# Kernel optimization log

Measured on AMD Instinct MI355X. Metric: run time of the kernel, lower is better.

## Reference

```python
import jax, jax.numpy as jnp
import numpy as np

N_FEAT = 256
N_HID = 128
N_HEAD = 4
N_HEAD_LAST = 6
N_CLASS = 40
NEG_SLOPE = 0.2


def gat_conv(x, src, dst, W, att_src, att_dst, bias, heads, ch, concat):
    # x: [N, in], W: [in, heads*ch], att_*: [heads, ch]
    N = x.shape[0]
    xw = (x @ W).reshape(N, heads, ch)                      # [N, H, C]
    a_src = jnp.sum(xw * att_src, axis=-1)                  # [N, H]
    a_dst = jnp.sum(xw * att_dst, axis=-1)                  # [N, H]
    e = jax.nn.leaky_relu(a_src[src] + a_dst[dst], NEG_SLOPE)  # [E, H]
    # softmax over incoming edges of each destination node
    m = jax.ops.segment_max(e, dst, num_segments=N)         # [N, H]
    ex = jnp.exp(e - m[dst])
    denom = jax.ops.segment_sum(ex, dst, num_segments=N)    # [N, H]
    alpha = ex / (denom[dst] + 1e-16)                       # [E, H]
    msg = xw[src] * alpha[..., None]                        # [E, H, C]
    out = jax.ops.segment_sum(msg, dst, num_segments=N)     # [N, H, C]
    out = out.reshape(N, heads * ch) if concat else out.mean(axis=1)
    return out + bias


def setup_inputs() -> dict:
    key = jax.random.key(0)
    ks = jax.random.split(key, 16)
    N, E = 10000, 160000
    x = jax.random.normal(ks[0], (N, N_FEAT), dtype=jnp.float32)
    edge_index = jax.random.randint(ks[1], (2, E), 0, N, dtype=jnp.int64)
    hid = N_HID * N_HEAD  # 512
    s = lambda fan: 1.0 / np.sqrt(fan)
    return {
        "x": x,
        "edge_index": edge_index,
        "W0": jax.random.normal(ks[2], (N_FEAT, hid), jnp.float32) * s(N_FEAT),
        "a_src0": jax.random.normal(ks[3], (N_HEAD, N_HID), jnp.float32) * s(N_HID),
        "a_dst0": jax.random.normal(ks[4], (N_HEAD, N_HID), jnp.float32) * s(N_HID),
        "b0": jnp.zeros((hid,), jnp.float32),
        "Wskip_in": jax.random.normal(ks[5], (N_FEAT, hid), jnp.float32) * s(N_FEAT),
        "W1": jax.random.normal(ks[6], (hid, hid), jnp.float32) * s(hid),
        "a_src1": jax.random.normal(ks[7], (N_HEAD, N_HID), jnp.float32) * s(N_HID),
        "a_dst1": jax.random.normal(ks[8], (N_HEAD, N_HID), jnp.float32) * s(N_HID),
        "b1": jnp.zeros((hid,), jnp.float32),
        "W2": jax.random.normal(ks[9], (hid, N_HEAD_LAST * N_CLASS), jnp.float32) * s(hid),
        "a_src2": jax.random.normal(ks[10], (N_HEAD_LAST, N_CLASS), jnp.float32) * s(N_CLASS),
        "a_dst2": jax.random.normal(ks[11], (N_HEAD_LAST, N_CLASS), jnp.float32) * s(N_CLASS),
        "b2": jnp.zeros((N_CLASS,), jnp.float32),
        "Wskip_out": jax.random.normal(ks[12], (hid, N_CLASS), jnp.float32) * s(hid),
    }


def reference(x, edge_index, W0, a_src0, a_dst0, b0, Wskip_in,
              W1, a_src1, a_dst1, b1,
              W2, a_src2, a_dst2, b2, Wskip_out):
    N = x.shape[0]
    loops = jnp.arange(N, dtype=edge_index.dtype)
    src = jnp.concatenate([edge_index[0], loops])  # add self loops (PyG GATConv)
    dst = jnp.concatenate([edge_index[1], loops])
    # eval mode: dropout is identity
    h = gat_conv(x, src, dst, W0, a_src0, a_dst0, b0, N_HEAD, N_HID, True)
    x1 = jax.nn.elu(h + x @ Wskip_in)                      # res skip w/ projection
    h = gat_conv(x1, src, dst, W1, a_src1, a_dst1, b1, N_HEAD, N_HID, True)
    x2 = jax.nn.elu(h + x1)                                # res skip, same dims
    h = gat_conv(x2, src, dst, W2, a_src2, a_dst2, b2, N_HEAD_LAST, N_CLASS, False)
    out = h + x2 @ Wskip_out                               # out_skip 'res'
    return out
```

## Files before the change

### kernel.cpp

```cpp
#include <hip/hip_runtime.h>
#include <math.h>


#define N_FEAT 256
#define HID 512

using u16 = unsigned short;
using bf16x8 = __attribute__((ext_vector_type(8))) __bf16;
using f32x16 = __attribute__((ext_vector_type(16))) float;

__device__ inline u16 bf16_rne(float f) {
    unsigned u = __float_as_uint(f);
    return (u16)((u + 0x7fffu + ((u >> 16) & 1u)) >> 16);
}
__device__ inline float bf16_to_f32(u16 h) {
    return __uint_as_float((unsigned)h << 16);
}
__device__ inline bf16x8 ldb8(const u16* p) {
    return *reinterpret_cast<const bf16x8*>(p);
}
__device__ inline void acc8(float a, const uint4 r, float* acc) {
    acc[0] = fmaf(a, __uint_as_float(r.x << 16), acc[0]);
    acc[1] = fmaf(a, __uint_as_float(r.x & 0xffff0000u), acc[1]);
    acc[2] = fmaf(a, __uint_as_float(r.y << 16), acc[2]);
    acc[3] = fmaf(a, __uint_as_float(r.y & 0xffff0000u), acc[3]);
    acc[4] = fmaf(a, __uint_as_float(r.z << 16), acc[4]);
    acc[5] = fmaf(a, __uint_as_float(r.z & 0xffff0000u), acc[5]);
    acc[6] = fmaf(a, __uint_as_float(r.w << 16), acc[6]);
    acc[7] = fmaf(a, __uint_as_float(r.w & 0xffff0000u), acc[7]);
}


__global__ void init_counts(int* cursor, int N) {
    int i = blockIdx.x * blockDim.x + threadIdx.x;
    if (i < N) cursor[i] = 1;
}

__global__ void count_edges(const int* __restrict__ ei, int E, int* cursor) {
    int e = blockIdx.x * blockDim.x + threadIdx.x;
    if (e < E) atomicAdd(&cursor[ei[E + e]], 1);
}

__global__ __launch_bounds__(1024) void scan_offsets(int* cursor, int* row_off, int N) {
    __shared__ int sdata[1024];
    int tid = threadIdx.x;
    int chunk = (N + 1023) >> 10;
    int base = tid * chunk;
    int lsum = 0;
    for (int i = 0; i < chunk; i++) {
        int idx = base + i;
        if (idx < N) lsum += cursor[idx];
    }
    sdata[tid] = lsum;
    __syncthreads();
    for (int off = 1; off < 1024; off <<= 1) {
        int t = (tid >= off) ? sdata[tid - off] : 0;
        __syncthreads();
        sdata[tid] += t;
        __syncthreads();
    }
    int run = sdata[tid] - lsum;
    if (tid == 0) row_off[0] = 0;
    for (int i = 0; i < chunk; i++) {
        int idx = base + i;
        if (idx < N) {
            int c = cursor[idx];
            cursor[idx] = run;
            run += c;
            row_off[idx + 1] = run;
        }
    }
}

__global__ void fill_csr(const int* __restrict__ ei, int E, int N,
                         int* cursor, int* __restrict__ col) {
    int i = blockIdx.x * blockDim.x + threadIdx.x;
    int tot = E + N;
    if (i >= tot) return;
    int s, d;
    if (i < E) { s = ei[i]; d = ei[E + i]; }
    else       { s = i - E; d = s; }
    int pos = atomicAdd(&cursor[d], 1);
    col[pos] = s;
}


__global__ __launch_bounds__(256) void att_combine_all(
        const float* __restrict__ W0, const float* __restrict__ as0, const float* __restrict__ ad0,
        const float* __restrict__ W1, const float* __restrict__ as1, const float* __restrict__ ad1,
        const float* __restrict__ W2, const float* __restrict__ as2, const float* __restrict__ ad2,
        float* __restrict__ ac0, float* __restrict__ ac1, float* __restrict__ ac2) {
    int i = blockIdx.x * blockDim.x + threadIdx.x;
    const float *W, *as_, *ad_;
    float* ac;
    int K, H, C, li;
    if (i < 2048)       { W = W0; as_ = as0; ad_ = ad0; ac = ac0; K = 256; H = 4; C = 128; li = i; }
    else if (i < 6144)  { W = W1; as_ = as1; ad_ = ad1; ac = ac1; K = 512; H = 4; C = 128; li = i - 2048; }
    else if (i < 12288) { W = W2; as_ = as2; ad_ = ad2; ac = ac2; K = 512; H = 6; C = 40;  li = i - 6144; }
    else return;
    int k = li / (2 * H);
    int hh = li - k * 2 * H;
    int h = (hh >= H) ? hh - H : hh;
    const float* av = ((hh >= H) ? ad_ : as_) + h * C;
    const float* wp = W + (size_t)k * H * C + (size_t)h * C;
    float sum = 0.f;
    for (int c = 0; c < C; c++) sum = fmaf(wp[c], av[c], sum);
    ac[(size_t)k * 2 * H + hh] = sum;
}


__global__ __launch_bounds__(256) void cvtA_pack(const float* __restrict__ X,
                                                 u16* __restrict__ hi, u16* __restrict__ lo,
                                                 int M, int K, int Rblocks) {
    int gid = blockIdx.x * blockDim.x + threadIdx.x;
    int lane = gid & 63;
    int rest = gid >> 6;
    int KC = K >> 4;
    int R = rest / KC;
    int c = rest - R * KC;
    if (R >= Rblocks) return;
    int row = R * 32 + (lane & 31);
    if (row >= M) row = M - 1;
    const float* src = X + (size_t)row * K + c * 16 + (lane >> 5) * 8;
    float4 v0 = *reinterpret_cast<const float4*>(src);
    float4 v1 = *reinterpret_cast<const float4*>(src + 4);
    float vv[8] = {v0.x, v0.y, v0.z, v0.w, v1.x, v1.y, v1.z, v1.w};
    unsigned hp[4], lp[4];
    #pragma unroll
    for (int j = 0; j < 4; j++) {
        u16 h0 = bf16_rne(vv[2 * j]);
        u16 h1 = bf16_rne(vv[2 * j + 1]);
        float r0 = vv[2 * j]     - __uint_as_float((unsigned)h0 << 16);
        float r1 = vv[2 * j + 1] - __uint_as_float((unsigned)h1 << 16);
        u16 l0 = bf16_rne(r0);
        u16 l1 = bf16_rne(r1);
        hp[j] = (unsigned)h0 | ((unsigned)h1 << 16);
        lp[j] = (unsigned)l0 | ((unsigned)l1 << 16);
    }
    size_t dst = ((size_t)rest * 64 + lane) * 8;
    *reinterpret_cast<int4*>(hi + dst) = make_int4(hp[0], hp[1], hp[2], hp[3]);
    *reinterpret_cast<int4*>(lo + dst) = make_int4(lp[0], lp[1], lp[2], lp[3]);
}

__device__ inline void cvtB_body(const float* __restrict__ B,
                                 u16* __restrict__ hi, u16* __restrict__ lo,
                                 int K, int Nb, int gid) {
    int lane = gid & 63;
    int rest = gid >> 6;
    int KC = K >> 4;
    int Cb = rest / KC;
    int c = rest - Cb * KC;
    int n = Cb * 32 + (lane & 31);
    int kbase = c * 16 + (lane >> 5) * 8;
    float vv[8];
    #pragma unroll
    for (int j = 0; j < 8; j++)
        vv[j] = (n < Nb) ? B[(size_t)(kbase + j) * Nb + n] : 0.f;
    unsigned hp[4], lp[4];
    #pragma unroll
    for (int j = 0; j < 4; j++) {
        u16 h0 = bf16_rne(vv[2 * j]);
        u16 h1 = bf16_rne(vv[2 * j + 1]);
        float r0 = vv[2 * j]     - __uint_as_float((unsigned)h0 << 16);
        float r1 = vv[2 * j + 1] - __uint_as_float((unsigned)h1 << 16);
        u16 l0 = bf16_rne(r0);
        u16 l1 = bf16_rne(r1);
        hp[j] = (unsigned)h0 | ((unsigned)h1 << 16);
        lp[j] = (unsigned)l0 | ((unsigned)l1 << 16);
    }
    size_t dst = ((size_t)rest * 64 + lane) * 8;
    *reinterpret_cast<int4*>(hi + dst) = make_int4(hp[0], hp[1], hp[2], hp[3]);
    *reinterpret_cast<int4*>(lo + dst) = make_int4(lp[0], lp[1], lp[2], lp[3]);
}

__global__ __launch_bounds__(256) void pack_all_B(
        const float* __restrict__ W0, const float* __restrict__ Wsi, const float* __restrict__ ac0,
        const float* __restrict__ W1, const float* __restrict__ ac1,
        const float* __restrict__ W2, const float* __restrict__ Wso, const float* __restrict__ ac2,
        u16* __restrict__ B0h, u16* __restrict__ B0l,
        u16* __restrict__ B1h, u16* __restrict__ B1l,
        u16* __restrict__ B2h, u16* __restrict__ B2l) {
    int g = blockIdx.x * blockDim.x + threadIdx.x;
    if (g < 16384)      cvtB_body(W0,  B0h, B0l, 256, 512, g);
    else if (g < 32768) cvtB_body(Wsi, B0h + (size_t)16 * 16 * 512, B0l + (size_t)16 * 16 * 512, 256, 512, g - 16384);
    else if (g < 34816) cvtB_body(ac0, B0h + (size_t)32 * 16 * 512, B0l + (size_t)32 * 16 * 512, 256, 8,   g - 32768);
    else if (g < 67584) cvtB_body(W1,  B1h, B1l, 512, 512, g - 34816);
    else if (g < 71680) cvtB_body(ac1, B1h + (size_t)16 * 32 * 512, B1l + (size_t)16 * 32 * 512, 512, 8,   g - 67584);
    else if (g < 88064) cvtB_body(W2,  B2h, B2l, 512, 240, g - 71680);
    else if (g < 92160) cvtB_body(Wso, B2h + (size_t)8 * 32 * 512,  B2l + (size_t)8 * 32 * 512,  512, 40,  g - 88064);
    else if (g < 96256) cvtB_body(ac2, B2h + (size_t)10 * 32 * 512, B2l + (size_t)10 * 32 * 512, 512, 12,  g - 92160);
}


__global__ __launch_bounds__(256) void gemm_fused(const u16* __restrict__ Ahi,
                                                  const u16* __restrict__ Alo,
                                                  const u16* __restrict__ Bhi,
                                                  const u16* __restrict__ Blo,
                                                  u16* __restrict__ xwb, int xwCols,
                                                  float* __restrict__ skipP,
                                                  int skipBeg, int skipEnd,
                                                  float* __restrict__ asrc,
                                                  float* __restrict__ adst,
                                                  int attBeg, int H,
                                                  int M, int K,
                                                  int ntiles, int Rblocks) {
    int nwg = gridDim.x, b = blockIdx.x;
    int q = nwg >> 3, r = nwg & 7;
    int xcd = b & 7, idx = b >> 3;
    int t = (xcd < r) ? (xcd * (q + 1) + idx)
                      : (r * (q + 1) + (xcd - r) * q + idx);
    int bm = (t / ntiles) * 128;
    int bn = (t - (t / ntiles) * ntiles) * 64;

    int lane = threadIdx.x & 63, w = threadIdx.x >> 6;
    int wr = w >> 1, wc = w & 1;
    int l31 = lane & 31, lg = lane >> 5;
    int KC = K >> 4;

    int R0 = (bm + wr * 64) >> 5;
    int R1 = R0 + 1;
    if (R0 >= Rblocks) R0 = Rblocks - 1;
    if (R1 >= Rblocks) R1 = Rblocks - 1;
    int Cb = (bn + wc * 32) >> 5;

    const u16* pa0h = Ahi + (((size_t)R0 * KC) * 64 + lane) * 8;
    const u16* pa0l = Alo + (((size_t)R0 * KC) * 64 + lane) * 8;
    const u16* pa1h = Ahi + (((size_t)R1 * KC) * 64 + lane) * 8;
    const u16* pa1l = Alo + (((size_t)R1 * KC) * 64 + lane) * 8;
    const u16* pbh  = Bhi + (((size_t)Cb * KC) * 64 + lane) * 8;
    const u16* pbl  = Blo + (((size_t)Cb * KC) * 64 + lane) * 8;

    f32x16 acc0, acc1;
    #pragma unroll
    for (int i2 = 0; i2 < 16; i2++) { acc0[i2] = 0.f; acc1[i2] = 0.f; }

    bf16x8 a0h = ldb8(pa0h), a0l = ldb8(pa0l);
    bf16x8 a1h = ldb8(pa1h), a1l = ldb8(pa1l);
    bf16x8 bh  = ldb8(pbh),  bl  = ldb8(pbl);

    for (int c = 1; c <= KC; c++) {
        size_t off = (size_t)c * 512;
        bf16x8 na0h = ldb8(pa0h + off), na0l = ldb8(pa0l + off);
        bf16x8 na1h = ldb8(pa1h + off), na1l = ldb8(pa1l + off);
        bf16x8 nbh  = ldb8(pbh + off),  nbl  = ldb8(pbl + off);
        acc0 = __builtin_amdgcn_mfma_f32_32x32x16_bf16(a0h, bh, acc0, 0, 0, 0);
        acc1 = __builtin_amdgcn_mfma_f32_32x32x16_bf16(a1h, bh, acc1, 0, 0, 0);
        acc0 = __builtin_amdgcn_mfma_f32_32x32x16_bf16(a0h, bl, acc0, 0, 0, 0);
        acc1 = __builtin_amdgcn_mfma_f32_32x32x16_bf16(a1h, bl, acc1, 0, 0, 0);
        acc0 = __builtin_amdgcn_mfma_f32_32x32x16_bf16(a0l, bh, acc0, 0, 0, 0);
        acc1 = __builtin_amdgcn_mfma_f32_32x32x16_bf16(a1l, bh, acc1, 0, 0, 0);
        a0h = na0h; a0l = na0l; a1h = na1h; a1l = na1l; bh = nbh; bl = nbl;
    }

    int n = bn + wc * 32 + l31;
    int base_m = bm + wr * 64;
    #pragma unroll
    for (int rg = 0; rg < 16; rg++) {
        int mrow = (rg & 3) + 8 * (rg >> 2) + 4 * lg;
        int m0 = base_m + mrow;
        int m1 = m0 + 32;
        float v0 = acc0[rg], v1 = acc1[rg];
        if (n < xwCols) {
            if (m0 < M) xwb[(size_t)m0 * xwCols + n] = bf16_rne(v0);
            if (m1 < M) xwb[(size_t)m1 * xwCols + n] = bf16_rne(v1);
        } else if (n >= skipBeg && n < skipEnd) {
            int cc = n - skipBeg, st = skipEnd - skipBeg;
            if (m0 < M) skipP[(size_t)m0 * st + cc] = v0;
            if (m1 < M) skipP[(size_t)m1 * st + cc] = v1;
        } else if (n >= attBeg && n < attBeg + H) {
            int h = n - attBeg;
            if (m0 < M) asrc[(size_t)m0 * H + h] = v0;
            if (m1 < M) asrc[(size_t)m1 * H + h] = v1;
        } else if (n >= attBeg + H && n < attBeg + 2 * H) {
            int h = n - attBeg - H;
            if (m0 < M) adst[(size_t)m0 * H + h] = v0;
            if (m1 < M) adst[(size_t)m1 * H + h] = v1;
        }
    }
}


template <int SKIPPK>
__global__ __launch_bounds__(256) void agg_sm512(const u16* __restrict__ xw,
                                                 const float* __restrict__ asrc,
                                                 const float* __restrict__ adst,
                                                 const int* __restrict__ row_off,
                                                 const int* __restrict__ col,
                                                 const float* __restrict__ bias,
                                                 const float* __restrict__ skipF,
                                                 const u16* __restrict__ skipHi,
                                                 const u16* __restrict__ skipLo,
                                                 u16* __restrict__ outHi,
                                                 u16* __restrict__ outLo,
                                                 int N) {
    __shared__ float lalpha[2][256 * 4];
    __shared__ int   lcol[2][256];
    __shared__ float lmerge[2][512];
    int tid = threadIdx.x;
    int widx = tid >> 6;
    int p = widx >> 1;
    int half = widx & 1;
    int lane = tid & 63;
    int w = blockIdx.x * 2 + p;
    bool valid = w < N;
    int jb = 0, je = 0;
    float adn[4], m[4], inv[4];

    if (valid) {
        jb = row_off[w]; je = row_off[w + 1];
        float4 ad4 = *reinterpret_cast<const float4*>(&adst[(size_t)w * 4]);
        adn[0] = ad4.x; adn[1] = ad4.y; adn[2] = ad4.z; adn[3] = ad4.w;

        float ev[4][4];
        int scol[4];
        #pragma unroll
        for (int h = 0; h < 4; h++) m[h] = -INFINITY;

        #pragma unroll
        for (int c = 0; c < 4; c++) {
            int j = jb + c * 64 + lane;
            if (j < je) {
                int s = col[j]; scol[c] = s;
                float4 as4 = *reinterpret_cast<const float4*>(&asrc[(size_t)s * 4]);
                float e0 = as4.x + adn[0]; e0 = e0 > 0.f ? e0 : 0.2f * e0;
                float e1 = as4.y + adn[1]; e1 = e1 > 0.f ? e1 : 0.2f * e1;
                float e2 = as4.z + adn[2]; e2 = e2 > 0.f ? e2 : 0.2f * e2;
                float e3 = as4.w + adn[3]; e3 = e3 > 0.f ? e3 : 0.2f * e3;
                ev[c][0] = e0; ev[c][1] = e1; ev[c][2] = e2; ev[c][3] = e3;
                m[0] = fmaxf(m[0], e0); m[1] = fmaxf(m[1], e1);
                m[2] = fmaxf(m[2], e2); m[3] = fmaxf(m[3], e3);
            } else {
                scol[c] = -1;
                #pragma unroll
                for (int h = 0; h < 4; h++) ev[c][h] = -INFINITY;
            }
        }
        for (int j = jb + 256 + lane; j < je; j += 64) {
            int s = col[j];
            #pragma unroll
            for (int h = 0; h < 4; h++) {
                float e = asrc[(size_t)s * 4 + h] + adn[h];
                e = e > 0.f ? e : 0.2f * e;
                m[h] = fmaxf(m[h], e);
            }
        }
        #pragma unroll
        for (int off = 32; off; off >>= 1)
            #pragma unroll
            for (int h = 0; h < 4; h++) m[h] = fmaxf(m[h], __shfl_xor(m[h], off));

        float ssum[4] = {0.f, 0.f, 0.f, 0.f};
        #pragma unroll
        for (int c = 0; c < 4; c++)
            #pragma unroll
            for (int h = 0; h < 4; h++) ssum[h] += __expf(ev[c][h] - m[h]);
        for (int j = jb + 256 + lane; j < je; j += 64) {
            int s = col[j];
            #pragma unroll
            for (int h = 0; h < 4; h++) {
                float e = asrc[(size_t)s * 4 + h] + adn[h];
                e = e > 0.f ? e : 0.2f * e;
                ssum[h] += __expf(e - m[h]);
            }
        }
        #pragma unroll
        for (int off = 32; off; off >>= 1)
            #pragma unroll
            for (int h = 0; h < 4; h++) ssum[h] += __shfl_xor(ssum[h], off);
        #pragma unroll
        for (int h = 0; h < 4; h++) inv[h] = 1.f / (ssum[h] + 1e-16f);

        #pragma unroll
        for (int c = 0; c < 4; c++) {
            int rel = c * 64 + lane;
            if (jb + rel < je) {
                lcol[p][rel] = scol[c];
                *reinterpret_cast<float4*>(&lalpha[p][rel * 4]) = make_float4(
                    __expf(ev[c][0] - m[0]) * inv[0],
                    __expf(ev[c][1] - m[1]) * inv[1],
                    __expf(ev[c][2] - m[2]) * inv[2],
                    __expf(ev[c][3] - m[3]) * inv[3]);
            }
        }
    }
    __syncthreads();

    int base = lane * 8;
    int hme = lane >> 4;
    float acc[8] = {};
    int deg = je - jb;
    int fast = deg < 256 ? deg : 256;

    if (valid) {
        int j = half;
        for (; j + 6 < fast; j += 8) {
            int s0 = lcol[p][j],     s1 = lcol[p][j + 2];
            int s2 = lcol[p][j + 4], s3 = lcol[p][j + 6];
            float a0 = lalpha[p][(j + 0) * 4 + hme];
            float a1 = lalpha[p][(j + 2) * 4 + hme];
            float a2 = lalpha[p][(j + 4) * 4 + hme];
            float a3 = lalpha[p][(j + 6) * 4 + hme];
            uint4 r0 = *reinterpret_cast<const uint4*>(&xw[(size_t)s0 * 512 + base]);
            uint4 r1 = *reinterpret_cast<const uint4*>(&xw[(size_t)s1 * 512 + base]);
            uint4 r2 = *reinterpret_cast<const uint4*>(&xw[(size_t)s2 * 512 + base]);
            uint4 r3 = *reinterpret_cast<const uint4*>(&xw[(size_t)s3 * 512 + base]);
            acc8(a0, r0, acc); acc8(a1, r1, acc);
            acc8(a2, r2, acc); acc8(a3, r3, acc);
        }
        for (; j < fast; j += 2) {
            int s = lcol[p][j];
            float a = lalpha[p][j * 4 + hme];
            uint4 raw = *reinterpret_cast<const uint4*>(&xw[(size_t)s * 512 + base]);
            acc8(a, raw, acc);
        }
        if (deg > 256 && half == 0) {
            for (int jj = jb + 256; jj < je; ++jj) {
                int s = col[jj];
                float e = asrc[(size_t)s * 4 + hme] + adn[hme];
                e = e > 0.f ? e : 0.2f * e;
                float a = __expf(e - m[hme]) * inv[hme];
                uint4 raw = *reinterpret_cast<const uint4*>(&xw[(size_t)s * 512 + base]);
                acc8(a, raw, acc);
            }
        }
        if (half == 1) {
            *reinterpret_cast<float4*>(&lmerge[p][base])     = make_float4(acc[0], acc[1], acc[2], acc[3]);
            *reinterpret_cast<float4*>(&lmerge[p][base + 4]) = make_float4(acc[4], acc[5], acc[6], acc[7]);
        }
    }
    __syncthreads();
    if (!valid || half == 1) return;

    {
        float4 m0 = *reinterpret_cast<const float4*>(&lmerge[p][base]);
        float4 m1 = *reinterpret_cast<const float4*>(&lmerge[p][base + 4]);
        acc[0] += m0.x; acc[1] += m0.y; acc[2] += m0.z; acc[3] += m0.w;
        acc[4] += m1.x; acc[5] += m1.y; acc[6] += m1.z; acc[7] += m1.w;
    }

    int R = w >> 5, r31 = w & 31, cc = lane >> 1, sub = lane & 1;
    int lp = r31 | (sub << 5);
    size_t slot = (((size_t)R * 32 + cc) * 64 + lp) * 8;

    float sk[8];
    if (SKIPPK) {
        int4 h4 = *reinterpret_cast<const int4*>(skipHi + slot);
        int4 l4 = *reinterpret_cast<const int4*>(skipLo + slot);
        unsigned hu[4] = {(unsigned)h4.x, (unsigned)h4.y, (unsigned)h4.z, (unsigned)h4.w};
        unsigned lu[4] = {(unsigned)l4.x, (unsigned)l4.y, (unsigned)l4.z, (unsigned)l4.w};
        #pragma unroll
        for (int i = 0; i < 4; i++) {
            sk[2 * i]     = __uint_as_float(hu[i] << 16) + __uint_as_float(lu[i] << 16);
            sk[2 * i + 1] = __uint_as_float(hu[i] & 0xffff0000u)
                          + __uint_as_float(lu[i] & 0xffff0000u);
        }
    } else {
        const float* kp = &skipF[(size_t)w * 512 + base];
        float4 s0 = *reinterpret_cast<const float4*>(kp);
        float4 s1 = *reinterpret_cast<const float4*>(kp + 4);
        sk[0] = s0.x; sk[1] = s0.y; sk[2] = s0.z; sk[3] = s0.w;
        sk[4] = s1.x; sk[5] = s1.y; sk[6] = s1.z; sk[7] = s1.w;
    }

    const float* bp = &bias[base];
    float r[8];
    #pragma unroll
    for (int i = 0; i < 8; i++) {
        float v = acc[i] + bp[i] + sk[i];
        r[i] = v > 0.f ? v : expm1f(v);
    }

    unsigned hp[4], lpk[4];
    #pragma unroll
    for (int i = 0; i < 4; i++) {
        u16 h0 = bf16_rne(r[2 * i]);
        u16 h1 = bf16_rne(r[2 * i + 1]);
        float q0 = r[2 * i]     - __uint_as_float((unsigned)h0 << 16);
        float q1 = r[2 * i + 1] - __uint_as_float((unsigned)h1 << 16);
        u16 l0 = bf16_rne(q0);
        u16 l1 = bf16_rne(q1);
        hp[i]  = (unsigned)h0 | ((unsigned)h1 << 16);
        lpk[i] = (unsigned)l0 | ((unsigned)l1 << 16);
    }
    *reinterpret_cast<int4*>(outHi + slot) = make_int4(hp[0], hp[1], hp[2], hp[3]);
    *reinterpret_cast<int4*>(outLo + slot) = make_int4(lpk[0], lpk[1], lpk[2], lpk[3]);
}


__global__ __launch_bounds__(256) void agg_final240_sm(const u16* __restrict__ xw,
                                                       const float* __restrict__ asrc,
                                                       const float* __restrict__ adst,
                                                       const int* __restrict__ row_off,
                                                       const int* __restrict__ col,
                                                       const float* __restrict__ b2,
                                                       const float* __restrict__ skip,
                                                       float* __restrict__ out,
                                                       int N) {
    __shared__ float lalpha[4][256 * 6];
    __shared__ int   lcol[4][256];
    __shared__ float lmerge[4][240];
    int w = (blockIdx.x * blockDim.x + threadIdx.x) >> 6;
    int lane = threadIdx.x & 63;
    int wid = (threadIdx.x >> 6) & 3;
    bool valid = w < N;
    int jb = 0, je = 0;
    float adn[6], m[6], inv[6];

    if (valid) {
        jb = row_off[w]; je = row_off[w + 1];
        #pragma unroll
        for (int h = 0; h < 6; h++) adn[h] = adst[(size_t)w * 6 + h];

        float ev[4][6];
        int scol[4];
        #pragma unroll
        for (int h = 0; h < 6; h++) m[h] = -INFINITY;

        #pragma unroll
        for (int c = 0; c < 4; c++) {
            int j = jb + c * 64 + lane;
            if (j < je) {
                int s = col[j]; scol[c] = s;
                #pragma unroll
                for (int h = 0; h < 6; h++) {
                    float e = asrc[(size_t)s * 6 + h] + adn[h];
                    e = e > 0.f ? e : 0.2f * e;
                    ev[c][h] = e;
                    m[h] = fmaxf(m[h], e);
                }
            } else {
                scol[c] = -1;
                #pragma unroll
                for (int h = 0; h < 6; h++) ev[c][h] = -INFINITY;
            }
        }
        for (int j = jb + 256 + lane; j < je; j += 64) {
            int s = col[j];
            #pragma unroll
            for (int h = 0; h < 6; h++) {
                float e = asrc[(size_t)s * 6 + h] + adn[h];
                e = e > 0.f ? e : 0.2f * e;
                m[h] = fmaxf(m[h], e);
            }
        }
        #pragma unroll
        for (int off = 32; off; off >>= 1)
            #pragma unroll
            for (int h = 0; h < 6; h++) m[h] = fmaxf(m[h], __shfl_xor(m[h], off));

        float ssum[6] = {0.f, 0.f, 0.f, 0.f, 0.f, 0.f};
        #pragma unroll
        for (int c = 0; c < 4; c++)
            #pragma unroll
            for (int h = 0; h < 6; h++) ssum[h] += __expf(ev[c][h] - m[h]);
        for (int j = jb + 256 + lane; j < je; j += 64) {
            int s = col[j];
            #pragma unroll
            for (int h = 0; h < 6; h++) {
                float e = asrc[(size_t)s * 6 + h] + adn[h];
                e = e > 0.f ? e : 0.2f * e;
                ssum[h] += __expf(e - m[h]);
            }
        }
        #pragma unroll
        for (int off = 32; off; off >>= 1)
            #pragma unroll
            for (int h = 0; h < 6; h++) ssum[h] += __shfl_xor(ssum[h], off);
        #pragma unroll
        for (int h = 0; h < 6; h++) inv[h] = 1.f / (ssum[h] + 1e-16f);

        #pragma unroll
        for (int c = 0; c < 4; c++) {
            int rel = c * 64 + lane;
            if (jb + rel < je) {
                lcol[wid][rel] = scol[c];
                #pragma unroll
                for (int h = 0; h < 6; h++)
                    lalpha[wid][rel * 6 + h] = __expf(ev[c][h] - m[h]) * inv[h];
            }
        }
    }
    __syncthreads();

    int h60 = lane / 10;
    int i10 = lane - h60 * 10;
    bool activeB = lane < 60;
    int coff = h60 * 40 + i10 * 4;
    float acc[4] = {};
    int deg = je - jb;
    int fast = deg < 256 ? deg : 256;

    if (valid && activeB) {
        int j = 0;
        for (; j + 3 < fast; j += 4) {
            int s0 = lcol[wid][j],     s1 = lcol[wid][j + 1];
            int s2 = lcol[wid][j + 2], s3 = lcol[wid][j + 3];
            float a0 = lalpha[wid][(j + 0) * 6 + h60];
            float a1 = lalpha[wid][(j + 1) * 6 + h60];
            float a2 = lalpha[wid][(j + 2) * 6 + h60];
            float a3 = lalpha[wid][(j + 3) * 6 + h60];
            uint2 r0 = *reinterpret_cast<const uint2*>(&xw[(size_t)s0 * 240 + coff]);
            uint2 r1 = *reinterpret_cast<const uint2*>(&xw[(size_t)s1 * 240 + coff]);
            uint2 r2 = *reinterpret_cast<const uint2*>(&xw[(size_t)s2 * 240 + coff]);
            uint2 r3 = *reinterpret_cast<const uint2*>(&xw[(size_t)s3 * 240 + coff]);
            acc[0] = fmaf(a0, __uint_as_float(r0.x << 16), acc[0]);
            acc[1] = fmaf(a0, __uint_as_float(r0.x & 0xffff0000u), acc[1]);
            acc[2] = fmaf(a0, __uint_as_float(r0.y << 16), acc[2]);
            acc[3] = fmaf(a0, __uint_as_float(r0.y & 0xffff0000u), acc[3]);
            acc[0] = fmaf(a1, __uint_as_float(r1.x << 16), acc[0]);
            acc[1] = fmaf(a1, __uint_as_float(r1.x & 0xffff0000u), acc[1]);
            acc[2] = fmaf(a1, __uint_as_float(r1.y << 16), acc[2]);
            acc[3] = fmaf(a1, __uint_as_float(r1.y & 0xffff0000u), acc[3]);
            acc[0] = fmaf(a2, __uint_as_float(r2.x << 16), acc[0]);
            acc[1] = fmaf(a2, __uint_as_float(r2.x & 0xffff0000u), acc[1]);
            acc[2] = fmaf(a2, __uint_as_float(r2.y << 16), acc[2]);
            acc[3] = fmaf(a2, __uint_as_float(r2.y & 0xffff0000u), acc[3]);
            acc[0] = fmaf(a3, __uint_as_float(r3.x << 16), acc[0]);
            acc[1] = fmaf(a3, __uint_as_float(r3.x & 0xffff0000u), acc[1]);
            acc[2] = fmaf(a3, __uint_as_float(r3.y << 16), acc[2]);
            acc[3] = fmaf(a3, __uint_as_float(r3.y & 0xffff0000u), acc[3]);
        }
        for (; j < fast; ++j) {
            int s = lcol[wid][j];
            float a = lalpha[wid][j * 6 + h60];
            uint2 raw = *reinterpret_cast<const uint2*>(&xw[(size_t)s * 240 + coff]);
            acc[0] = fmaf(a, __uint_as_float(raw.x << 16), acc[0]);
            acc[1] = fmaf(a, __uint_as_float(raw.x & 0xffff0000u), acc[1]);
            acc[2] = fmaf(a, __uint_as_float(raw.y << 16), acc[2]);
            acc[3] = fmaf(a, __uint_as_float(raw.y & 0xffff0000u), acc[3]);
        }
        if (deg > 256) {
            for (int jj = jb + 256; jj < je; ++jj) {
                int s = col[jj];
                float e = asrc[(size_t)s * 6 + h60] + adn[h60];
                e = e > 0.f ? e : 0.2f * e;
                float a = __expf(e - m[h60]) * inv[h60];
                uint2 raw = *reinterpret_cast<const uint2*>(&xw[(size_t)s * 240 + coff]);
                acc[0] = fmaf(a, __uint_as_float(raw.x << 16), acc[0]);
                acc[1] = fmaf(a, __uint_as_float(raw.x & 0xffff0000u), acc[1]);
                acc[2] = fmaf(a, __uint_as_float(raw.y << 16), acc[2]);
                acc[3] = fmaf(a, __uint_as_float(raw.y & 0xffff0000u), acc[3]);
            }
        }
        *reinterpret_cast<float4*>(&lmerge[wid][lane * 4]) =
            make_float4(acc[0], acc[1], acc[2], acc[3]);
    }
    __syncthreads();
    if (!valid) return;

    if (lane < 40) {
        float s = 0.f;
        #pragma unroll
        for (int h = 0; h < 6; h++) s += lmerge[wid][h * 40 + lane];
        float v = s * (1.f / 6.f) + b2[lane] + skip[(size_t)w * 40 + lane];
        out[(size_t)w * 40 + lane] = v;
    }
}


extern "C" void kernel_launch(void* const* d_in, const int* in_sizes, int n_in,
                              void* d_out, int out_size, void* d_ws, size_t ws_size,
                              hipStream_t stream) {
    const float* x        = (const float*)d_in[0];
    const int*   ei       = (const int*)  d_in[1];
    const float* W0       = (const float*)d_in[2];
    const float* a_src0   = (const float*)d_in[3];
    const float* a_dst0   = (const float*)d_in[4];
    const float* b0       = (const float*)d_in[5];
    const float* Wskip_in = (const float*)d_in[6];
    const float* W1       = (const float*)d_in[7];
    const float* a_src1   = (const float*)d_in[8];
    const float* a_dst1   = (const float*)d_in[9];
    const float* b1       = (const float*)d_in[10];
    const float* W2       = (const float*)d_in[11];
    const float* a_src2   = (const float*)d_in[12];
    const float* a_dst2   = (const float*)d_in[13];
    const float* b2       = (const float*)d_in[14];
    const float* Wskip_out= (const float*)d_in[15];

    const int N = in_sizes[0] / N_FEAT;
    const int E = in_sizes[1] / 2;
    float* out = (float*)d_out;

    const int Rblocks = (N + 31) / 32;
    const int mtiles = (N + 127) / 128;

    float* ws = (float*)d_ws;
    size_t o = 0;
    u16* xwb   = (u16*)(ws + o); o += (size_t)N * 256;
    float* tmpD  = ws + o; o += (size_t)N * HID;
    float* asrc  = ws + o; o += (size_t)N * 8;
    float* adst  = ws + o; o += (size_t)N * 8;
    float* skipo = ws + o; o += (size_t)N * 40;
    float* ac0   = ws + o; o += 256 * 8;
    float* ac1   = ws + o; o += 512 * 8;
    float* ac2   = ws + o; o += 512 * 12;

    u16* up = (u16*)(ws + o);
    size_t uo = 0;
    const size_t aPack = (size_t)Rblocks * 32 * 512 + 512;
    u16* AhA = up + uo; uo += aPack;   u16* AlA = up + uo; uo += aPack;
    u16* AhB = up + uo; uo += aPack;   u16* AlB = up + uo; uo += aPack;
    const size_t b0sz = (size_t)34 * 16 * 512 + 512;
    u16* B0h = up + uo; uo += b0sz;  u16* B0l = up + uo; uo += b0sz;
    const size_t b1sz = (size_t)18 * 32 * 512 + 512;
    u16* B1h = up + uo; uo += b1sz;  u16* B1l = up + uo; uo += b1sz;
    const size_t b2sz = (size_t)12 * 32 * 512 + 512;
    u16* B2h = up + uo; uo += b2sz;  u16* B2l = up + uo; uo += b2sz;
    int* row_off = (int*)(up + uo);
    int* cursor  = row_off + (N + 1);
    int* col     = cursor + (N + 1);

    init_counts<<<(N + 255) / 256, 256, 0, stream>>>(cursor, N);
    count_edges<<<(E + 255) / 256, 256, 0, stream>>>(ei, E, cursor);
    scan_offsets<<<1, 1024, 0, stream>>>(cursor, row_off, N);
    fill_csr<<<(E + N + 255) / 256, 256, 0, stream>>>(ei, E, N, cursor, col);

    att_combine_all<<<48, 256, 0, stream>>>(W0, a_src0, a_dst0,
                                            W1, a_src1, a_dst1,
                                            W2, a_src2, a_dst2, ac0, ac1, ac2);
    pack_all_B<<<376, 256, 0, stream>>>(W0, Wskip_in, ac0, W1, ac1,
                                        W2, Wskip_out, ac2,
                                        B0h, B0l, B1h, B1l, B2h, B2l);

    int pairBlocks = (N + 1) / 2;
    int nodeBlocks = (N * 64 + 255) / 256;
    const int BIG = 1 << 30;

    cvtA_pack<<<(Rblocks * 16 * 64 + 255) / 256, 256, 0, stream>>>(x, AhA, AlA, N, 256, Rblocks);
    gemm_fused<<<mtiles * 17, 256, 0, stream>>>(
        AhA, AlA, B0h, B0l, xwb, 512, tmpD, 512, 1024, asrc, adst, 1024, 4,
        N, 256, 17, Rblocks);
    agg_sm512<0><<<pairBlocks, 256, 0, stream>>>(
        xwb, asrc, adst, row_off, col, b0, tmpD, nullptr, nullptr, AhB, AlB, N);

    gemm_fused<<<mtiles * 9, 256, 0, stream>>>(
        AhB, AlB, B1h, B1l, xwb, 512, nullptr, BIG, BIG, asrc, adst, 512, 4,
        N, 512, 9, Rblocks);
    agg_sm512<1><<<pairBlocks, 256, 0, stream>>>(
        xwb, asrc, adst, row_off, col, b1, nullptr, AhB, AlB, AhA, AlA, N);

    gemm_fused<<<mtiles * 6, 256, 0, stream>>>(
        AhA, AlA, B2h, B2l, xwb, 240, skipo, 256, 296, asrc, adst, 320, 6,
        N, 512, 6, Rblocks);
    agg_final240_sm<<<nodeBlocks, 256, 0, stream>>>(
        xwb, asrc, adst, row_off, col, b2, skipo, out, N);
}
```

Measured before the change: 345.7 us.

## Widen GEMM tile to 128x128 and use one wave per node in aggregation

Each GEMM wave now computes a 64x64 output block from four accumulators instead of 64x32, so every A fragment load feeds twice as many MFMAs and the grid shrinks by about half. The packed B buffers are padded so the column count is a multiple of 128. The 512-wide aggregation kernel now assigns one wave per destination node, four nodes per block, and drops the two-wave edge split along with its shared-memory merge and second barrier. Costs: more accumulator registers per thread and therefore possibly lower occupancy, some wasted MFMA work on padded columns, and less per-node parallelism for high-degree nodes.

```diff
diff --git a/kernel.cpp b/kernel.cpp
--- a/kernel.cpp
+++ b/kernel.cpp
@@ -181,36 +181,36 @@
         u16* __restrict__ B1h, u16* __restrict__ B1l,
         u16* __restrict__ B2h, u16* __restrict__ B2l) {
     int g = blockIdx.x * blockDim.x + threadIdx.x;
-    if (g < 16384)      cvtB_body(W0,  B0h, B0l, 256, 512, g);
-    else if (g < 32768) cvtB_body(Wsi, B0h + (size_t)16 * 16 * 512, B0l + (size_t)16 * 16 * 512, 256, 512, g - 16384);
-    else if (g < 34816) cvtB_body(ac0, B0h + (size_t)32 * 16 * 512, B0l + (size_t)32 * 16 * 512, 256, 8,   g - 32768);
-    else if (g < 67584) cvtB_body(W1,  B1h, B1l, 512, 512, g - 34816);
-    else if (g < 71680) cvtB_body(ac1, B1h + (size_t)16 * 32 * 512, B1l + (size_t)16 * 32 * 512, 512, 8,   g - 67584);
-    else if (g < 88064) cvtB_body(W2,  B2h, B2l, 512, 240, g - 71680);
-    else if (g < 92160) cvtB_body(Wso, B2h + (size_t)8 * 32 * 512,  B2l + (size_t)8 * 32 * 512,  512, 40,  g - 88064);
-    else if (g < 96256) cvtB_body(ac2, B2h + (size_t)10 * 32 * 512, B2l + (size_t)10 * 32 * 512, 512, 12,  g - 92160);
-}
-
-
-__global__ __launch_bounds__(256) void gemm_fused(const u16* __restrict__ Ahi,
-                                                  const u16* __restrict__ Alo,
-                                                  const u16* __restrict__ Bhi,
-                                                  const u16* __restrict__ Blo,
-                                                  u16* __restrict__ xwb, int xwCols,
-                                                  float* __restrict__ skipP,
-                                                  int skipBeg, int skipEnd,
-                                                  float* __restrict__ asrc,
-                                                  float* __restrict__ adst,
-                                                  int attBeg, int H,
-                                                  int M, int K,
-                                                  int ntiles, int Rblocks) {
+    if (g < 16384)       cvtB_body(W0,  B0h, B0l, 256, 512, g);
+    else if (g < 32768)  cvtB_body(Wsi, B0h + (size_t)16 * 16 * 512, B0l + (size_t)16 * 16 * 512, 256, 512, g - 16384);
+    else if (g < 36864)  cvtB_body(ac0, B0h + (size_t)32 * 16 * 512, B0l + (size_t)32 * 16 * 512, 256, 8,   g - 32768);
+    else if (g < 69632)  cvtB_body(W1,  B1h, B1l, 512, 512, g - 36864);
+    else if (g < 77824)  cvtB_body(ac1, B1h + (size_t)16 * 32 * 512, B1l + (size_t)16 * 32 * 512, 512, 8,   g - 69632);
+    else if (g < 94208)  cvtB_body(W2,  B2h, B2l, 512, 240, g - 77824);
+    else if (g < 98304)  cvtB_body(Wso, B2h + (size_t)8 * 32 * 512,  B2l + (size_t)8 * 32 * 512,  512, 40,  g - 94208);
+    else if (g < 102400) cvtB_body(ac2, B2h + (size_t)10 * 32 * 512, B2l + (size_t)10 * 32 * 512, 512, 12,  g - 98304);
+}
+
+
+__global__ __launch_bounds__(256) void gemm_fused2(const u16* __restrict__ Ahi,
+                                                   const u16* __restrict__ Alo,
+                                                   const u16* __restrict__ Bhi,
+                                                   const u16* __restrict__ Blo,
+                                                   u16* __restrict__ xwb, int xwCols,
+                                                   float* __restrict__ skipP,
+                                                   int skipBeg, int skipEnd,
+                                                   float* __restrict__ asrc,
+                                                   float* __restrict__ adst,
+                                                   int attBeg, int H,
+                                                   int M, int K,
+                                                   int ntiles, int Rblocks) {
     int nwg = gridDim.x, b = blockIdx.x;
     int q = nwg >> 3, r = nwg & 7;
     int xcd = b & 7, idx = b >> 3;
     int t = (xcd < r) ? (xcd * (q + 1) + idx)
                       : (r * (q + 1) + (xcd - r) * q + idx);
     int bm = (t / ntiles) * 128;
-    int bn = (t - (t / ntiles) * ntiles) * 64;
+    int bn = (t - (t / ntiles) * ntiles) * 128;
 
     int lane = threadIdx.x & 63, w = threadIdx.x >> 6;
     int wr = w >> 1, wc = w & 1;
@@ -221,60 +221,77 @@
     int R1 = R0 + 1;
     if (R0 >= Rblocks) R0 = Rblocks - 1;
     if (R1 >= Rblocks) R1 = Rblocks - 1;
-    int Cb = (bn + wc * 32) >> 5;
+    int C0 = (bn + wc * 64) >> 5;
+    int C1 = C0 + 1;
 
     const u16* pa0h = Ahi + (((size_t)R0 * KC) * 64 + lane) * 8;
     const u16* pa0l = Alo + (((size_t)R0 * KC) * 64 + lane) * 8;
     const u16* pa1h = Ahi + (((size_t)R1 * KC) * 64 + lane) * 8;
     const u16* pa1l = Alo + (((size_t)R1 * KC) * 64 + lane) * 8;
-    const u16* pbh  = Bhi + (((size_t)Cb * KC) * 64 + lane) * 8;
-    const u16* pbl  = Blo + (((size_t)Cb * KC) * 64 + lane) * 8;
-
-    f32x16 acc0, acc1;
+    const u16* pb0h = Bhi + (((size_t)C0 * KC) * 64 + lane) * 8;
+    const u16* pb0l = Blo + (((size_t)C0 * KC) * 64 + lane) * 8;
+    const u16* pb1h = Bhi + (((size_t)C1 * KC) * 64 + lane) * 8;
+    const u16* pb1l = Blo + (((size_t)C1 * KC) * 64 + lane) * 8;
+
+    f32x16 acc00, acc01, acc10, acc11;
     #pragma unroll
-    for (int i2 = 0; i2 < 16; i2++) { acc0[i2] = 0.f; acc1[i2] = 0.f; }
+    for (int i2 = 0; i2 < 16; i2++) {
+        acc00[i2] = 0.f; acc01[i2] = 0.f; acc10[i2] = 0.f; acc11[i2] = 0.f;
+    }
 
     bf16x8 a0h = ldb8(pa0h), a0l = ldb8(pa0l);
     bf16x8 a1h = ldb8(pa1h), a1l = ldb8(pa1l);
-    bf16x8 bh  = ldb8(pbh),  bl  = ldb8(pbl);
+    bf16x8 b0h = ldb8(pb0h), b0l = ldb8(pb0l);
+    bf16x8 b1h = ldb8(pb1h), b1l = ldb8(pb1l);
 
     for (int c = 1; c <= KC; c++) {
         size_t off = (size_t)c * 512;
         bf16x8 na0h = ldb8(pa0h + off), na0l = ldb8(pa0l + off);
         bf16x8 na1h = ldb8(pa1h + off), na1l = ldb8(pa1l + off);
-        bf16x8 nbh  = ldb8(pbh + off),  nbl  = ldb8(pbl + off);
-        acc0 = __builtin_amdgcn_mfma_f32_32x32x16_bf16(a0h, bh, acc0, 0, 0, 0);
-        acc1 = __builtin_amdgcn_mfma_f32_32x32x16_bf16(a1h, bh, acc1, 0, 0, 0);
-        acc0 = __builtin_amdgcn_mfma_f32_32x32x16_bf16(a0h, bl, acc0, 0, 0, 0);
-        acc1 = __builtin_amdgcn_mfma_f32_32x32x16_bf16(a1h, bl, acc1, 0, 0, 0);
-        acc0 = __builtin_amdgcn_mfma_f32_32x32x16_bf16(a0l, bh, acc0, 0, 0, 0);
-        acc1 = __builtin_amdgcn_mfma_f32_32x32x16_bf16(a1l, bh, acc1, 0, 0, 0);
-        a0h = na0h; a0l = na0l; a1h = na1h; a1l = na1l; bh = nbh; bl = nbl;
-    }
-
-    int n = bn + wc * 32 + l31;
+        bf16x8 nb0h = ldb8(pb0h + off), nb0l = ldb8(pb0l + off);
+        bf16x8 nb1h = ldb8(pb1h + off), nb1l = ldb8(pb1l + off);
+        acc00 = __builtin_amdgcn_mfma_f32_32x32x16_bf16(a0h, b0h, acc00, 0, 0, 0);
+        acc01 = __builtin_amdgcn_mfma_f32_32x32x16_bf16(a0h, b1h, acc01, 0, 0, 0);
+        acc10 = __builtin_amdgcn_mfma_f32_32x32x16_bf16(a1h, b0h, acc10, 0, 0, 0);
+        acc11 = __builtin_amdgcn_mfma_f32_32x32x16_bf16(a1h, b1h, acc11, 0, 0, 0);
+        acc00 = __builtin_amdgcn_mfma_f32_32x32x16_bf16(a0h, b0l, acc00, 0, 0, 0);
+        acc01 = __builtin_amdgcn_mfma_f32_32x32x16_bf16(a0h, b1l, acc01, 0, 0, 0);
+        acc10 = __builtin_amdgcn_mfma_f32_32x32x16_bf16(a1h, b0l, acc10, 0, 0, 0);
+        acc11 = __builtin_amdgcn_mfma_f32_32x32x16_bf16(a1h, b1l, acc11, 0, 0, 0);
+        acc00 = __builtin_amdgcn_mfma_f32_32x32x16_bf16(a0l, b0h, acc00, 0, 0, 0);
+        acc01 = __builtin_amdgcn_mfma_f32_32x32x16_bf16(a0l, b1h, acc01, 0, 0, 0);
+        acc10 = __builtin_amdgcn_mfma_f32_32x32x16_bf16(a1l, b0h, acc10, 0, 0, 0);
+        acc11 = __builtin_amdgcn_mfma_f32_32x32x16_bf16(a1l, b1h, acc11, 0, 0, 0);
+        a0h = na0h; a0l = na0l; a1h = na1h; a1l = na1l;
+        b0h = nb0h; b0l = nb0l; b1h = nb1h; b1l = nb1l;
+    }
+
+    int n0 = bn + wc * 64 + l31;
+    int n1 = n0 + 32;
     int base_m = bm + wr * 64;
+
     #pragma unroll
     for (int rg = 0; rg < 16; rg++) {
         int mrow = (rg & 3) + 8 * (rg >> 2) + 4 * lg;
         int m0 = base_m + mrow;
         int m1 = m0 + 32;
-        float v0 = acc0[rg], v1 = acc1[rg];
-        if (n < xwCols) {
-            if (m0 < M) xwb[(size_t)m0 * xwCols + n] = bf16_rne(v0);
-            if (m1 < M) xwb[(size_t)m1 * xwCols + n] = bf16_rne(v1);
-        } else if (n >= skipBeg && n < skipEnd) {
-            int cc = n - skipBeg, st = skipEnd - skipBeg;
-            if (m0 < M) skipP[(size_t)m0 * st + cc] = v0;
-            if (m1 < M) skipP[(size_t)m1 * st + cc] = v1;
-        } else if (n >= attBeg && n < attBeg + H) {
-            int h = n - attBeg;
-            if (m0 < M) asrc[(size_t)m0 * H + h] = v0;
-            if (m1 < M) asrc[(size_t)m1 * H + h] = v1;
-        } else if (n >= attBeg + H && n < attBeg + 2 * H) {
-            int h = n - attBeg - H;
-            if (m0 < M) adst[(size_t)m0 * H + h] = v0;
-            if (m1 < M) adst[(size_t)m1 * H + h] = v1;
+        float v00 = acc00[rg], v01 = acc01[rg];
+        float v10 = acc10[rg], v11 = acc11[rg];
+        #pragma unroll
+        for (int pp = 0; pp < 4; pp++) {
+            int m = (pp & 2) ? m1 : m0;
+            int n = (pp & 1) ? n1 : n0;
+            float v = (pp == 0) ? v00 : (pp == 1) ? v01 : (pp == 2) ? v10 : v11;
+            if (m >= M) continue;
+            if (n < xwCols) {
+                xwb[(size_t)m * xwCols + n] = bf16_rne(v);
+            } else if (n >= skipBeg && n < skipEnd) {
+                skipP[(size_t)m * (skipEnd - skipBeg) + (n - skipBeg)] = v;
+            } else if (n >= attBeg && n < attBeg + H) {
+                asrc[(size_t)m * H + (n - attBeg)] = v;
+            } else if (n >= attBeg + H && n < attBeg + 2 * H) {
+                adst[(size_t)m * H + (n - attBeg - H)] = v;
+            }
         }
     }
 }
@@ -293,15 +310,11 @@
                                                  u16* __restrict__ outHi,
                                                  u16* __restrict__ outLo,
                                                  int N) {
-    __shared__ float lalpha[2][256 * 4];
-    __shared__ int   lcol[2][256];
-    __shared__ float lmerge[2][512];
-    int tid = threadIdx.x;
-    int widx = tid >> 6;
-    int p = widx >> 1;
-    int half = widx & 1;
-    int lane = tid & 63;
-    int w = blockIdx.x * 2 + p;
+    __shared__ float lalpha[4][256 * 4];
+    __shared__ int   lcol[4][256];
+    int w = (blockIdx.x * blockDim.x + threadIdx.x) >> 6;
+    int lane = threadIdx.x & 63;
+    int wid = (threadIdx.x >> 6) & 3;
     bool valid = w < N;
     int jb = 0, je = 0;
     float adn[4], m[4], inv[4];
@@ -374,8 +387,8 @@
         for (int c = 0; c < 4; c++) {
             int rel = c * 64 + lane;
             if (jb + rel < je) {
-                lcol[p][rel] = scol[c];
-                *reinterpret_cast<float4*>(&lalpha[p][rel * 4]) = make_float4(
+                lcol[wid][rel] = scol[c];
+                *reinterpret_cast<float4*>(&lalpha[wid][rel * 4]) = make_float4(
                     __expf(ev[c][0] - m[0]) * inv[0],
                     __expf(ev[c][1] - m[1]) * inv[1],
                     __expf(ev[c][2] - m[2]) * inv[2],
@@ -384,6 +397,7 @@
         }
     }
     __syncthreads();
+    if (!valid) return;
 
     int base = lane * 8;
     int hme = lane >> 4;
@@ -391,51 +405,38 @@
     int deg = je - jb;
     int fast = deg < 256 ? deg : 256;
 
-    if (valid) {
-        int j = half;
-        for (; j + 6 < fast; j += 8) {
-            int s0 = lcol[p][j],     s1 = lcol[p][j + 2];
-            int s2 = lcol[p][j + 4], s3 = lcol[p][j + 6];
-            float a0 = lalpha[p][(j + 0) * 4 + hme];
-            float a1 = lalpha[p][(j + 2) * 4 + hme];
-            float a2 = lalpha[p][(j + 4) * 4 + hme];
-            float a3 = lalpha[p][(j + 6) * 4 + hme];
-            uint4 r0 = *reinterpret_cast<const uint4*>(&xw[(size_t)s0 * 512 + base]);
-            uint4 r1 = *reinterpret_cast<const uint4*>(&xw[(size_t)s1 * 512 + base]);
-            uint4 r2 = *reinterpret_cast<const uint4*>(&xw[(size_t)s2 * 512 + base]);
-            uint4 r3 = *reinterpret_cast<const uint4*>(&xw[(size_t)s3 * 512 + base]);
-            acc8(a0, r0, acc); acc8(a1, r1, acc);
-            acc8(a2, r2, acc); acc8(a3, r3, acc);
-        }
-        for (; j < fast; j += 2) {
-            int s = lcol[p][j];
-            float a = lalpha[p][j * 4 + hme];
+    int j = 0;
+    for (; j + 3 < fast; j += 4) {
+        int4 cs = *reinterpret_cast<const int4*>(&lcol[wid][j]);
+        float a0 = lalpha[wid][(j + 0) * 4 + hme];
+        float a1 = lalpha[wid][(j + 1) * 4 + hme];
+        float a2 = lalpha[wid][(j + 2) * 4 + hme];
+        float a3 = lalpha[wid][(j + 3) * 4 + hme];
+        uint4 r0 = *reinterpret_cast<const uint4*>(&xw[(size_t)cs.x * 512 + base]);
+        uint4 r1 = *reinterpret_cast<const uint4*>(&xw[(size_t)cs.y * 512 + base]);
+        uint4 r2 = *reinterpret_cast<const uint4*>(&xw[(size_t)cs.z * 512 + base]);
+        uint4 r3 = *reinterpret_cast<const uint4*>(&xw[(size_t)cs.w * 512 + base]);
+        acc8(a0, r0, acc); acc8(a1, r1, acc);
+        acc8(a2, r2, acc); acc8(a3, r3, acc);
+    }
+    for (; j < fast; ++j) {
+        int s = lcol[wid][j];
+        float a = lalpha[wid][j * 4 + hme];
+        uint4 raw = *reinterpret_cast<const uint4*>(&xw[(size_t)s * 512 + base]);
+        acc8(a, raw, acc);
+    }
+    if (deg > 256) {
+        float adn_h = hme == 0 ? adn[0] : hme == 1 ? adn[1] : hme == 2 ? adn[2] : adn[3];
+        float m_h   = hme == 0 ? m[0]   : hme == 1 ? m[1]   : hme == 2 ? m[2]   : m[3];
+        float inv_h = hme == 0 ? inv[0] : hme == 1 ? inv[1] : hme == 2 ? inv[2] : inv[3];
+        for (int jj = jb + 256; jj < je; ++jj) {
+            int s = col[jj];
+            float e = asrc[(size_t)s * 4 + hme] + adn_h;
+            e = e > 0.f ? e : 0.2f * e;
+            float a = __expf(e - m_h) * inv_h;
             uint4 raw = *reinterpret_cast<const uint4*>(&xw[(size_t)s * 512 + base]);
             acc8(a, raw, acc);
         }
-        if (deg > 256 && half == 0) {
-            for (int jj = jb + 256; jj < je; ++jj) {
-                int s = col[jj];
-                float e = asrc[(size_t)s * 4 + hme] + adn[hme];
-                e = e > 0.f ? e : 0.2f * e;
-                float a = __expf(e - m[hme]) * inv[hme];
-                uint4 raw = *reinterpret_cast<const uint4*>(&xw[(size_t)s * 512 + base]);
-                acc8(a, raw, acc);
-            }
-        }
-        if (half == 1) {
-            *reinterpret_cast<float4*>(&lmerge[p][base])     = make_float4(acc[0], acc[1], acc[2], acc[3]);
-            *reinterpret_cast<float4*>(&lmerge[p][base + 4]) = make_float4(acc[4], acc[5], acc[6], acc[7]);
-        }
-    }
-    __syncthreads();
-    if (!valid || half == 1) return;
-
-    {
-        float4 m0 = *reinterpret_cast<const float4*>(&lmerge[p][base]);
-        float4 m1 = *reinterpret_cast<const float4*>(&lmerge[p][base + 4]);
-        acc[0] += m0.x; acc[1] += m0.y; acc[2] += m0.z; acc[3] += m0.w;
-        acc[4] += m1.x; acc[5] += m1.y; acc[6] += m1.z; acc[7] += m1.w;
     }
 
     int R = w >> 5, r31 = w & 31, cc = lane >> 1, sub = lane & 1;
@@ -701,9 +702,9 @@
     const size_t aPack = (size_t)Rblocks * 32 * 512 + 512;
     u16* AhA = up + uo; uo += aPack;   u16* AlA = up + uo; uo += aPack;
     u16* AhB = up + uo; uo += aPack;   u16* AlB = up + uo; uo += aPack;
-    const size_t b0sz = (size_t)34 * 16 * 512 + 512;
+    const size_t b0sz = (size_t)36 * 16 * 512 + 512;
     u16* B0h = up + uo; uo += b0sz;  u16* B0l = up + uo; uo += b0sz;
-    const size_t b1sz = (size_t)18 * 32 * 512 + 512;
+    const size_t b1sz = (size_t)20 * 32 * 512 + 512;
     u16* B1h = up + uo; uo += b1sz;  u16* B1l = up + uo; uo += b1sz;
     const size_t b2sz = (size_t)12 * 32 * 512 + 512;
     u16* B2h = up + uo; uo += b2sz;  u16* B2l = up + uo; uo += b2sz;
@@ -719,30 +720,29 @@
     att_combine_all<<<48, 256, 0, stream>>>(W0, a_src0, a_dst0,
                                             W1, a_src1, a_dst1,
                                             W2, a_src2, a_dst2, ac0, ac1, ac2);
-    pack_all_B<<<376, 256, 0, stream>>>(W0, Wskip_in, ac0, W1, ac1,
+    pack_all_B<<<400, 256, 0, stream>>>(W0, Wskip_in, ac0, W1, ac1,
                                         W2, Wskip_out, ac2,
                                         B0h, B0l, B1h, B1l, B2h, B2l);
 
-    int pairBlocks = (N + 1) / 2;
     int nodeBlocks = (N * 64 + 255) / 256;
     const int BIG = 1 << 30;
 
     cvtA_pack<<<(Rblocks * 16 * 64 + 255) / 256, 256, 0, stream>>>(x, AhA, AlA, N, 256, Rblocks);
-    gemm_fused<<<mtiles * 17, 256, 0, stream>>>(
+    gemm_fused2<<<mtiles * 9, 256, 0, stream>>>(
         AhA, AlA, B0h, B0l, xwb, 512, tmpD, 512, 1024, asrc, adst, 1024, 4,
-        N, 256, 17, Rblocks);
-    agg_sm512<0><<<pairBlocks, 256, 0, stream>>>(
+        N, 256, 9, Rblocks);
+    agg_sm512<0><<<nodeBlocks, 256, 0, stream>>>(
         xwb, asrc, adst, row_off, col, b0, tmpD, nullptr, nullptr, AhB, AlB, N);
 
-    gemm_fused<<<mtiles * 9, 256, 0, stream>>>(
+    gemm_fused2<<<mtiles * 5, 256, 0, stream>>>(
         AhB, AlB, B1h, B1l, xwb, 512, nullptr, BIG, BIG, asrc, adst, 512, 4,
-        N, 512, 9, Rblocks);
-    agg_sm512<1><<<pairBlocks, 256, 0, stream>>>(
+        N, 512, 5, Rblocks);
+    agg_sm512<1><<<nodeBlocks, 256, 0, stream>>>(
         xwb, asrc, adst, row_off, col, b1, nullptr, AhB, AlB, AhA, AlA, N);
 
-    gemm_fused<<<mtiles * 6, 256, 0, stream>>>(
+    gemm_fused2<<<mtiles * 3, 256, 0, stream>>>(
         AhA, AlA, B2h, B2l, xwb, 240, skipo, 256, 296, asrc, adst, 320, 6,
-        N, 512, 6, Rblocks);
+        N, 512, 3, Rblocks);
     agg_final240_sm<<<nodeBlocks, 256, 0, stream>>>(
         xwb, asrc, adst, row_off, col, b2, skipo, out, N);
 }
```

Result: slower. 362.2 us (+4.8%).
